# Kernel tuning notes

Hardware: AMD Instinct MI355X
Metric: run time of the kernel (lower is better)

The kernel has to match this reference:

```python
import jax, jax.numpy as jnp
import numpy as np

NUM_HEADS = 12


def _attend(q, k, v, scale):
    # q: [B,H,Q,D], k/v: [B,H,K,D]
    attn = jnp.einsum('bhqd,bhkd->bhqk', q, k) * scale
    attn = jax.nn.softmax(attn, axis=-1)
    return jnp.einsum('bhqk,bhkd->bhqd', attn, v)


def setup_inputs() -> dict:
    key = jax.random.key(0)
    k1, k2, k3 = jax.random.split(key, 3)
    B, N, C = 32, 1009, 768
    x = jax.random.normal(k1, (B, N, C), dtype=jnp.float32)
    W_qkv = jax.random.normal(k2, (C, 3 * C), dtype=jnp.float32) * (C ** -0.5)
    b_qkv = jnp.zeros((3 * C,), dtype=jnp.float32)
    W_proj = jax.random.normal(k3, (C, C), dtype=jnp.float32) * (C ** -0.5)
    b_proj = jnp.zeros((C,), dtype=jnp.float32)
    return {"x": x, "W_qkv": W_qkv, "b_qkv": b_qkv, "W_proj": W_proj,
            "b_proj": b_proj, "query_len": 1, "lens_z": 432}


def reference(x, W_qkv, b_qkv, W_proj, b_proj, query_len, lens_z):
    B, N, C = x.shape
    H = NUM_HEADS
    D = C // H
    scale = D ** -0.5
    lens_x = N - query_len - lens_z

    qkv = (x @ W_qkv + b_qkv).reshape(B, N, 3, H, D)
    qkv = jnp.transpose(qkv, (2, 0, 3, 1, 4))  # [3,B,H,N,D]
    q, k, v = qkv[0], qkv[1], qkv[2]

    sl_p = slice(0, query_len)
    sl_t = slice(query_len, query_len + lens_z)
    sl_s = slice(query_len + lens_z, N)

    # prompt: local self-attention
    x_prompt = _attend(q[:, :, sl_p], k[:, :, sl_p], v[:, :, sl_p], scale)
    # template: local self-attention
    x_template = _attend(q[:, :, sl_t], k[:, :, sl_t], v[:, :, sl_t], scale)
    # search: global attention over all tokens
    x_search = _attend(q[:, :, sl_s], k, v, scale)

    def merge(y, L):
        return jnp.transpose(y, (0, 2, 1, 3)).reshape(B, L, C)

    out = jnp.concatenate([merge(x_prompt, query_len),
                           merge(x_template, lens_z),
                           merge(x_search, lens_x)], axis=1)
    return out @ W_proj + b_proj
```

## Files before the change

kernel.cpp:

```cpp
#include <hip/hip_runtime.h>

#define B_ 32
#define N_ 1009
#define C_ 768
#define H_ 12
#define D_ 64
#define M_ (B_*N_)
#define MT_ 253
#define MPAD_ (MT_*128)
#define NKV_ 1024

typedef __attribute__((ext_vector_type(4))) float f32x4;
typedef __attribute__((ext_vector_type(8))) short s16x8;

__device__ __forceinline__ unsigned short f2bf(float f) {
  union { float f; unsigned u; } x; x.f = f;
  unsigned r = x.u + 0x7fffu + ((x.u >> 16) & 1u);
  return (unsigned short)(r >> 16);
}

__device__ __forceinline__ f32x4 mfma16(s16x8 a, s16x8 b, f32x4 c) {
  return __builtin_amdgcn_mfma_f32_16x16x32_bf16(a, b, c, 0, 0, 0);
}

__device__ __forceinline__ void async16(const void* g, void* l) {
  __builtin_amdgcn_global_load_lds((const __attribute__((address_space(1))) void*)g,
                                   (__attribute__((address_space(3))) void*)l, 16, 0, 0);
}

__device__ __forceinline__ float exp2_fast(float x) {
  float r; asm("v_exp_f32 %0, %1" : "=v"(r) : "v"(x)); return r;
}

__device__ __forceinline__ unsigned cvt_pk_bf16(float lo, float hi) {
  unsigned r; asm("v_cvt_pk_bf16_f32 %0, %1, %2" : "=v"(r) : "v"(lo), "v"(hi)); return r;
}

template<int NWG>
__device__ __forceinline__ int xcd_swz(int bid) {
  constexpr int q = NWG >> 3, r = NWG & 7;
  const int x = bid & 7, l = bid >> 3;
  return (x < r ? x * (q + 1) : r * (q + 1) + (x - r) * q) + l;
}

__global__ void prep(const float* __restrict__ x, unsigned short* __restrict__ xb,
                     const float* __restrict__ W_qkv, unsigned short* __restrict__ wqkvT,
                     const float* __restrict__ W_proj, unsigned short* __restrict__ wprojT,
                     unsigned short* __restrict__ kb, unsigned short* __restrict__ vt) {
  __shared__ float tile[64][65];
  int blk = blockIdx.x;

  if (blk < 12144) {
    const long e = ((long)blk * 256 + threadIdx.x) * 8;
    const long row = e / 768;
    s16x8 v;
    if (row < M_) {
#pragma unroll
      for (int j = 0; j < 8; ++j) v[j] = (short)f2bf(x[e + j]);
    } else {
      v = (s16x8){0,0,0,0,0,0,0,0};
    }
    *(s16x8*)&xb[e] = v;
    return;
  }
  blk -= 12144;

  if (blk < 432 + 144) {
    const float* in;
    unsigned short* out;
    int R, Ccols, bx, by;
    if (blk < 432) { in = W_qkv;  out = wqkvT;  R = 768; Ccols = 2304; bx = blk % 36;  by = blk / 36; }
    else { const int b2 = blk - 432;
           in = W_proj; out = wprojT; R = 768; Ccols = 768;  bx = b2 % 12;   by = b2 / 12; }
    const int tc = bx * 64, tr = by * 64;
#pragma unroll
    for (int i = 0; i < 16; ++i) {
      const int e = i * 256 + threadIdx.x;
      const int r = e >> 6, c = e & 63;
      tile[r][c] = in[(long)(tr + r) * Ccols + tc + c];
    }
    __syncthreads();
#pragma unroll
    for (int i = 0; i < 16; ++i) {
      const int e = i * 256 + threadIdx.x;
      const int c = e >> 6, r = e & 63;
      out[(long)(tc + c) * R + tr + r] = f2bf(tile[r][c]);
    }
    return;
  }
  blk -= 576;

  const int t = blk * 256 + threadIdx.x;
  if (t >= 368640) return;
  const int d = t & 63;
  const int r = t >> 6;
  const int bh = r / 15, tok = 1009 + (r - bh * 15);
  kb[(((long)bh << 10) + tok) * 64 + d] = 0;
  const int c = t % 15, row = t / 15;
  vt[((long)row << 10) + 1009 + c] = 0;
}

template<int MODE>
__global__ __launch_bounds__(256, 3)
void gemm_bt(const unsigned short* __restrict__ A,
             const unsigned short* __restrict__ Bt,
             const float* __restrict__ bias,
             unsigned short* __restrict__ qo,
             unsigned short* __restrict__ ko,
             unsigned short* __restrict__ vo,
             float* __restrict__ fo) {
  __shared__ __align__(16) unsigned short smem[24576];
  const int tid = threadIdx.x;
  const int lane = tid & 63;
  const int wv = tid >> 6;
  constexpr int NBN = (MODE == 0) ? 18 : 6;
  const int swzid = xcd_swz<MT_ * NBN>(blockIdx.x);
  const int bm = swzid / NBN;
  const int bn = swzid - bm * NBN;
  const int row0 = bm * 128;
  const int col0 = bn * 128;
  const int wr = (wv >> 1) * 64;
  const int wc = (wv & 1) * 64;

  auto stage = [&](int slot, int kt) {
#pragma unroll
    for (int c = 0; c < 2; ++c) {
      const int lds_off = c * 4096 + wv * 1024;
      const int gg = c * 256 + wv * 64 + lane;
      const int row = gg >> 2;
      const int ck = ((gg & 3) ^ ((row >> 1) & 3)) << 3;
      async16(A + (long)(row0 + row) * 768 + kt + ck, (char*)smem + slot * 16384 + lds_off);
      async16(Bt + (long)(col0 + row) * 768 + kt + ck, (char*)smem + slot * 16384 + 8192 + lds_off);
    }
  };

  f32x4 acc[4][4] = {};
  stage(0, 0);
  stage(1, 32);
  for (int it = 0; it < 24; ++it) {
    const int sl = it % 3;
    if (it + 1 < 24) {
      asm volatile("s_waitcnt vmcnt(4)" ::: "memory");
    } else {
      asm volatile("s_waitcnt vmcnt(0)" ::: "memory");
    }
    __builtin_amdgcn_s_barrier();
    if (it + 2 < 24) stage((it + 2) % 3, (it + 2) * 32);

    const unsigned short* Asb = smem + sl * 8192;
    const unsigned short* Bsb = Asb + 4096;
    s16x8 af[4], bfr[4];
#pragma unroll
    for (int m = 0; m < 4; ++m) {
      const int rA = wr + m * 16 + (lane & 15);
      af[m] = *(const s16x8*)&Asb[rA * 32 + (((lane >> 4) ^ ((rA >> 1) & 3)) << 3)];
    }
#pragma unroll
    for (int n = 0; n < 4; ++n) {
      const int rB = wc + n * 16 + (lane & 15);
      bfr[n] = *(const s16x8*)&Bsb[rB * 32 + (((lane >> 4) ^ ((rB >> 1) & 3)) << 3)];
    }
    __builtin_amdgcn_s_setprio(1);
#pragma unroll
    for (int m = 0; m < 4; ++m)
#pragma unroll
      for (int n = 0; n < 4; ++n)
        acc[m][n] = mfma16(af[m], bfr[n], acc[m][n]);
    __builtin_amdgcn_s_setprio(0);
  }
  __syncthreads();

  if (MODE == 0 && col0 < 1536) {
    const int qsel = col0 < 768;
#pragma unroll
    for (int m = 0; m < 4; ++m)
#pragma unroll
      for (int j = 0; j < 4; ++j)
#pragma unroll
        for (int n = 0; n < 4; ++n) {
          const int tk = wr + m * 16 + (lane >> 4) * 4 + j;
          const int cl = wc + n * 16 + (lane & 15);
          float val = acc[m][n][j] + bias[col0 + cl];
          if (qsel) val *= 0.18033688011112042f;
          smem[tk * 136 + cl] = f2bf(val);
        }
    __syncthreads();
    unsigned short* const dst = qsel ? qo : ko;
    const int colb = col0 - (qsel ? 0 : 768);
#pragma unroll
    for (int it = 0; it < 8; ++it) {
      const int g = it * 256 + tid;
      const int tk = g >> 4;
      const int ch = (g & 15) * 8;
      const int grow = row0 + tk;
      if (grow < M_) {
        const s16x8 vv = *(const s16x8*)&smem[tk * 136 + ch];
        const int b = grow / N_;
        const int ntok = grow - b * N_;
        const int rem = colb + ch;
        const int h = rem >> 6, d = rem & 63;
        *(s16x8*)&dst[(((((long)b * H_ + h) << 10) + ntok) << 6) + d] = vv;
      }
    }
    return;
  }

  if (MODE == 0) {
#pragma unroll
    for (int m = 0; m < 4; ++m)
#pragma unroll
      for (int j = 0; j < 4; ++j)
#pragma unroll
        for (int n = 0; n < 4; ++n) {
          const int dl = wc + n * 16 + (lane & 15);
          const int tk = wr + m * 16 + (lane >> 4) * 4 + j;
          smem[dl * 136 + tk] = f2bf(acc[m][n][j] + bias[col0 + dl]);
        }
    __syncthreads();
    const int h0 = (col0 - 1536) >> 6;
    const int b0 = row0 / N_;
    const int split = (b0 + 1) * N_ - row0;
#pragma unroll
    for (int it = 0; it < 8; ++it) {
      const int g = it * 256 + tid;
      const int dl = g >> 4;
      const int t8 = (g & 15) * 8;
      const s16x8 vv = *(const s16x8*)&smem[dl * 136 + t8];
      const int hh = h0 + (dl >> 6), dd = dl & 63;
#pragma unroll
      for (int jj = 0; jj < 8; ++jj) {
        const int tkb = t8 + jj;
        const int grow = row0 + tkb;
        if (grow < M_) {
          const int bb = (tkb < split) ? b0 : b0 + 1;
          const int ntok = grow - bb * N_;
          vo[(((((long)bb * H_ + hh) << 6) + dd) << 10) + ntok] = (unsigned short)vv[jj];
        }
      }
    }
    return;
  }

#pragma unroll
  for (int m = 0; m < 4; ++m) {
#pragma unroll
    for (int j = 0; j < 4; ++j) {
      const int grow = row0 + wr + m * 16 + (lane >> 4) * 4 + j;
      if (grow < M_) {
#pragma unroll
        for (int n = 0; n < 4; ++n) {
          const int col = col0 + wc + n * 16 + (lane & 15);
          fo[(long)grow * 768 + col] = acc[m][n][j] + bias[col];
        }
      }
    }
  }
}

__global__ __launch_bounds__(256, 4)
void attn_kernel(const unsigned short* __restrict__ qg,
                 const unsigned short* __restrict__ kg,
                 const unsigned short* __restrict__ vtg,
                 unsigned short* __restrict__ og) {
  __shared__ __align__(16) unsigned short Ks[2][64 * 64];
  __shared__ __align__(16) unsigned short Vts[2][64 * 64];
  __shared__ __align__(16) unsigned short Ps[64 * 64];

  const int bid = blockIdx.x;
  const int swz = (bid & 7) * 768 + (bid >> 3);
  const int tile = swz & 15;
  const int bh = swz >> 4;
  const int b = bh / H_;
  const int h = bh - b * H_;
  int qbase, qend, kstart, ktiles, kend;
  if (tile < 7) { qbase = 1 + 64 * tile;       qend = 433;  kstart = 1; ktiles = 7;  kend = 433; }
  else          { qbase = 433 + 64 * (tile-7); qend = 1009; kstart = 0; ktiles = 16; kend = 1009; }
  const long base  = (long)bh << 10;
  const long vbase = (long)bh << 6;
  const int tid = threadIdx.x, lane = tid & 63, wv = tid >> 6;
  const int q15 = lane & 15, q7 = lane & 7, g = lane >> 4;

  if (tile == 7 && tid < 64)
    og[((long)b * N_) * 768 + h * 64 + tid] = vtg[(vbase + tid) << 10];

  s16x8 qa[2];
  {
    const unsigned short* qp = qg + (base + qbase + wv * 16 + q15) * 64;
    qa[0] = *(const s16x8*)(qp + g * 8);
    qa[1] = *(const s16x8*)(qp + 32 + g * 8);
  }
  asm volatile("s_waitcnt vmcnt(0)" ::: "memory");

  f32x4 o[4] = {};
  float mrow = -1e30f, lrow = 0.f;

  auto stage = [&](int bufsel, int kb0) {
#pragma unroll
    for (int it = 0; it < 2; ++it) {
      const int ldsoff = (it * 256 + wv * 64) * 16;
      const int gr = it * 256 + wv * 64 + lane;
      const int rl = gr >> 3;
      const int cs = (gr & 7) ^ (rl & 7);
      async16(kg + ((base + kb0 + rl) << 6) + cs * 8, (char*)&Ks[bufsel][0] + ldsoff);
      async16(vtg + ((vbase + rl) << 10) + kb0 + cs * 8, (char*)&Vts[bufsel][0] + ldsoff);
    }
  };

  const int prow = wv * 16 + q15;

  stage(0, kstart);
  for (int kt = 0; kt < ktiles; ++kt) {
    const int buf = kt & 1;
    const int kbase0 = kstart + 64 * kt;
    if (kt + 1 < ktiles) {
      stage(buf ^ 1, kbase0 + 64);
      asm volatile("s_waitcnt vmcnt(4)" ::: "memory");
    } else {
      asm volatile("s_waitcnt vmcnt(0)" ::: "memory");
    }
    __builtin_amdgcn_s_barrier();

    f32x4 s4[4];
    __builtin_amdgcn_s_setprio(1);
#pragma unroll
    for (int n = 0; n < 4; ++n) {
      const int krow = n * 16 + q15;
      const int r7 = krow & 7;
      f32x4 a = {};
      a = mfma16(*(const s16x8*)&Ks[buf][krow * 64 + ((g ^ r7) << 3)],       qa[0], a);
      a = mfma16(*(const s16x8*)&Ks[buf][krow * 64 + (((4 + g) ^ r7) << 3)], qa[1], a);
      s4[n] = a;
    }
    __builtin_amdgcn_s_setprio(0);

    if (kbase0 + 64 > kend) {
#pragma unroll
      for (int n = 0; n < 4; ++n)
#pragma unroll
        for (int j = 0; j < 4; ++j)
          if (kbase0 + n * 16 + g * 4 + j >= kend) s4[n][j] = -1e30f;
    }

    float rmax = fmaxf(
        fmaxf(fmaxf(fmaxf(s4[0][0], s4[0][1]), fmaxf(s4[0][2], s4[0][3])),
              fmaxf(fmaxf(s4[1][0], s4[1][1]), fmaxf(s4[1][2], s4[1][3]))),
        fmaxf(fmaxf(fmaxf(s4[2][0], s4[2][1]), fmaxf(s4[2][2], s4[2][3])),
              fmaxf(fmaxf(s4[3][0], s4[3][1]), fmaxf(s4[3][2], s4[3][3]))));
    rmax = fmaxf(rmax, __shfl_xor(rmax, 16));
    rmax = fmaxf(rmax, __shfl_xor(rmax, 32));

    if (!__all(rmax <= mrow + 8.f)) {
      const float mnew = fmaxf(mrow, rmax);
      const float corr = exp2_fast(mrow - mnew);
      mrow = mnew;
      lrow *= corr;
#pragma unroll
      for (int f = 0; f < 4; ++f)
#pragma unroll
        for (int j = 0; j < 4; ++j) o[f][j] *= corr;
    }
    const float mnew = mrow;

    float psum = 0.f;
#pragma unroll
    for (int n = 0; n < 4; ++n) {
#pragma unroll
      for (int j = 0; j < 4; ++j) {
        s4[n][j] = exp2_fast(s4[n][j] - mnew);
        psum += s4[n][j];
      }
      uint2 pw;
      pw.x = cvt_pk_bf16(s4[n][0], s4[n][1]);
      pw.y = cvt_pk_bf16(s4[n][2], s4[n][3]);
      *(uint2*)((char*)Ps + prow * 128 + (((n * 2 + (g >> 1)) ^ q7) << 4) + (g & 1) * 8) = pw;
    }
    psum += __shfl_xor(psum, 16);
    psum += __shfl_xor(psum, 32);
    lrow += psum;

    s16x8 pa[2];
#pragma unroll
    for (int kf = 0; kf < 2; ++kf)
      pa[kf] = *(const s16x8*)((char*)Ps + prow * 128 + (((kf * 4 + g) ^ q7) << 4));
    __builtin_amdgcn_s_setprio(1);
#pragma unroll
    for (int f = 0; f < 4; ++f) {
      const int vrow = f * 16 + q15;
      const int v7 = vrow & 7;
#pragma unroll
      for (int kf = 0; kf < 2; ++kf) {
        const s16x8 vb = *(const s16x8*)&Vts[buf][vrow * 64 + (((kf * 4 + g) ^ v7) << 3)];
        o[f] = mfma16(vb, pa[kf], o[f]);
      }
    }
    __builtin_amdgcn_s_setprio(0);

    asm volatile("s_waitcnt lgkmcnt(0)" ::: "memory");
    __builtin_amdgcn_s_barrier();
  }

  const int qrow = qbase + wv * 16 + q15;
  if (qrow < qend) {
    const float inv = 1.0f / lrow;
    unsigned short* op = og + ((long)b * N_ + qrow) * 768 + h * 64 + g * 4;
#pragma unroll
    for (int f = 0; f < 4; ++f) {
      uint2 ow;
      ow.x = cvt_pk_bf16(o[f][0] * inv, o[f][1] * inv);
      ow.y = cvt_pk_bf16(o[f][2] * inv, o[f][3] * inv);
      *(uint2*)(op + f * 16) = ow;
    }
  }
}

extern "C" void kernel_launch(void* const* d_in, const int* in_sizes, int n_in,
                              void* d_out, int out_size, void* d_ws, size_t ws_size,
                              hipStream_t stream) {
  const float* x      = (const float*)d_in[0];
  const float* W_qkv  = (const float*)d_in[1];
  const float* b_qkv  = (const float*)d_in[2];
  const float* W_proj = (const float*)d_in[3];
  const float* b_proj = (const float*)d_in[4];
  float* out = (float*)d_out;

  unsigned short* ws = (unsigned short*)d_ws;
  unsigned short* wqkvT  = ws;
  unsigned short* wprojT = wqkvT + (long)2304 * 768;
  unsigned short* qb = wprojT + (long)768 * 768;
  const long kvsz = (long)B_ * H_ * NKV_ * D_;
  unsigned short* kb = qb + kvsz;
  unsigned short* vb = kb + kvsz;
  unsigned short* xb = vb + kvsz;
  unsigned short* attnout = xb;

  prep<<<14160, 256, 0, stream>>>(x, xb, W_qkv, wqkvT, W_proj, wprojT, kb, vb);
  gemm_bt<0><<<MT_ * 18, 256, 0, stream>>>(xb, wqkvT, b_qkv, qb, kb, vb, nullptr);
  attn_kernel<<<B_ * H_ * 16, 256, 0, stream>>>(qb, kb, vb, attnout);
  gemm_bt<1><<<MT_ * 6, 256, 0, stream>>>(attnout, wprojT, b_proj, nullptr, nullptr, nullptr, out);
}
```

Before: 393.6 us.

## Process two query tiles per attention block to share K/V tile loads

Each attention workgroup now handles two 64-row query tiles against the same staged K/V tiles, which halves K/V global loads and LDS staging per query. The grid shrinks from 16 to 9 blocks per (batch, head). Odd tile counts are covered by having the last slot compute the same tile twice and write identical results. The cost is doubled accumulator and Q registers, some redundant compute on the duplicated tiles, and fewer blocks available to fill the GPU.

```diff
diff --git a/kernel.cpp b/kernel.cpp
--- a/kernel.cpp
+++ b/kernel.cpp
@@ -267,32 +267,39 @@
   __shared__ __align__(16) unsigned short Ps[64 * 64];
 
   const int bid = blockIdx.x;
-  const int swz = (bid & 7) * 768 + (bid >> 3);
-  const int tile = swz & 15;
-  const int bh = swz >> 4;
+  const int swz = (bid & 7) * 432 + (bid >> 3);
+  const int bh = swz / 9;
+  const int slot = swz - bh * 9;
   const int b = bh / H_;
   const int h = bh - b * H_;
-  int qbase, qend, kstart, ktiles, kend;
-  if (tile < 7) { qbase = 1 + 64 * tile;       qend = 433;  kstart = 1; ktiles = 7;  kend = 433; }
-  else          { qbase = 433 + 64 * (tile-7); qend = 1009; kstart = 0; ktiles = 16; kend = 1009; }
+  int kstart, ktiles, kend, qt0, qt1;
+  if (slot < 4) { kstart = 1; ktiles = 7;  kend = 433;
+                  qt0 = slot * 2;      qt1 = (slot < 3) ? qt0 + 1 : 6; }
+  else          { kstart = 0; ktiles = 16; kend = 1009; const int s2 = slot - 4;
+                  qt0 = 7 + s2 * 2;    qt1 = (s2 < 4) ? qt0 + 1 : 15; }
+  const int qb0 = (qt0 < 7) ? 1 + 64 * qt0 : 433 + 64 * (qt0 - 7);
+  const int qb1 = (qt1 < 7) ? 1 + 64 * qt1 : 433 + 64 * (qt1 - 7);
   const long base  = (long)bh << 10;
   const long vbase = (long)bh << 6;
   const int tid = threadIdx.x, lane = tid & 63, wv = tid >> 6;
   const int q15 = lane & 15, q7 = lane & 7, g = lane >> 4;
 
-  if (tile == 7 && tid < 64)
+  if (slot == 4 && tid < 64)
     og[((long)b * N_) * 768 + h * 64 + tid] = vtg[(vbase + tid) << 10];
 
-  s16x8 qa[2];
+  s16x8 qa0[2], qa1[2];
   {
-    const unsigned short* qp = qg + (base + qbase + wv * 16 + q15) * 64;
-    qa[0] = *(const s16x8*)(qp + g * 8);
-    qa[1] = *(const s16x8*)(qp + 32 + g * 8);
+    const unsigned short* qp0 = qg + (base + qb0 + wv * 16 + q15) * 64;
+    qa0[0] = *(const s16x8*)(qp0 + g * 8);
+    qa0[1] = *(const s16x8*)(qp0 + 32 + g * 8);
+    const unsigned short* qp1 = qg + (base + qb1 + wv * 16 + q15) * 64;
+    qa1[0] = *(const s16x8*)(qp1 + g * 8);
+    qa1[1] = *(const s16x8*)(qp1 + 32 + g * 8);
   }
   asm volatile("s_waitcnt vmcnt(0)" ::: "memory");
 
-  f32x4 o[4] = {};
-  float mrow = -1e30f, lrow = 0.f;
+  f32x4 o0[4] = {}, o1[4] = {};
+  float m0 = -1e30f, l0 = 0.f, m1 = -1e30f, l1 = 0.f;
 
   auto stage = [&](int bufsel, int kb0) {
 #pragma unroll
@@ -307,6 +314,84 @@
   };
 
   const int prow = wv * 16 + q15;
+
+  auto half = [&](const s16x8* qa, f32x4* o, float& mrow, float& lrow,
+                  int buf, int kbase0) {
+    f32x4 s4[4];
+    __builtin_amdgcn_s_setprio(1);
+#pragma unroll
+    for (int n = 0; n < 4; ++n) {
+      const int krow = n * 16 + q15;
+      const int r7 = krow & 7;
+      f32x4 a = {};
+      a = mfma16(*(const s16x8*)&Ks[buf][krow * 64 + ((g ^ r7) << 3)],       qa[0], a);
+      a = mfma16(*(const s16x8*)&Ks[buf][krow * 64 + (((4 + g) ^ r7) << 3)], qa[1], a);
+      s4[n] = a;
+    }
+    __builtin_amdgcn_s_setprio(0);
+
+    if (kbase0 + 64 > kend) {
+#pragma unroll
+      for (int n = 0; n < 4; ++n)
+#pragma unroll
+        for (int j = 0; j < 4; ++j)
+          if (kbase0 + n * 16 + g * 4 + j >= kend) s4[n][j] = -1e30f;
+    }
+
+    float rmax = fmaxf(
+        fmaxf(fmaxf(fmaxf(s4[0][0], s4[0][1]), fmaxf(s4[0][2], s4[0][3])),
+              fmaxf(fmaxf(s4[1][0], s4[1][1]), fmaxf(s4[1][2], s4[1][3]))),
+        fmaxf(fmaxf(fmaxf(s4[2][0], s4[2][1]), fmaxf(s4[2][2], s4[2][3])),
+              fmaxf(fmaxf(s4[3][0], s4[3][1]), fmaxf(s4[3][2], s4[3][3]))));
+    rmax = fmaxf(rmax, __shfl_xor(rmax, 16));
+    rmax = fmaxf(rmax, __shfl_xor(rmax, 32));
+
+    if (!__all(rmax <= mrow + 8.f)) {
+      const float mnew = fmaxf(mrow, rmax);
+      const float corr = exp2_fast(mrow - mnew);
+      mrow = mnew;
+      lrow *= corr;
+#pragma unroll
+      for (int f = 0; f < 4; ++f)
+#pragma unroll
+        for (int j = 0; j < 4; ++j) o[f][j] *= corr;
+    }
+    const float mnew = mrow;
+
+    float psum = 0.f;
+#pragma unroll
+    for (int n = 0; n < 4; ++n) {
+#pragma unroll
+      for (int j = 0; j < 4; ++j) {
+        s4[n][j] = exp2_fast(s4[n][j] - mnew);
+        psum += s4[n][j];
+      }
+      uint2 pw;
+      pw.x = cvt_pk_bf16(s4[n][0], s4[n][1]);
+      pw.y = cvt_pk_bf16(s4[n][2], s4[n][3]);
+      *(uint2*)((char*)Ps + prow * 128 + (((n * 2 + (g >> 1)) ^ q7) << 4) + (g & 1) * 8) = pw;
+    }
+    psum += __shfl_xor(psum, 16);
+    psum += __shfl_xor(psum, 32);
+    lrow += psum;
+
+    s16x8 pa[2];
+#pragma unroll
+    for (int kf = 0; kf < 2; ++kf)
+      pa[kf] = *(const s16x8*)((char*)Ps + prow * 128 + (((kf * 4 + g) ^ q7) << 4));
+    __builtin_amdgcn_s_setprio(1);
+#pragma unroll
+    for (int f = 0; f < 4; ++f) {
+      const int vrow = f * 16 + q15;
+      const int v7 = vrow & 7;
+#pragma unroll
+      for (int kf = 0; kf < 2; ++kf) {
+        const s16x8 vb = *(const s16x8*)&Vts[buf][vrow * 64 + (((kf * 4 + g) ^ v7) << 3)];
+        o[f] = mfma16(vb, pa[kf], o[f]);
+      }
+    }
+    __builtin_amdgcn_s_setprio(0);
+  };
 
   stage(0, kstart);
   for (int kt = 0; kt < ktiles; ++kt) {
@@ -320,95 +405,39 @@
     }
     __builtin_amdgcn_s_barrier();
 
-    f32x4 s4[4];
-    __builtin_amdgcn_s_setprio(1);
-#pragma unroll
-    for (int n = 0; n < 4; ++n) {
-      const int krow = n * 16 + q15;
-      const int r7 = krow & 7;
-      f32x4 a = {};
-      a = mfma16(*(const s16x8*)&Ks[buf][krow * 64 + ((g ^ r7) << 3)],       qa[0], a);
-      a = mfma16(*(const s16x8*)&Ks[buf][krow * 64 + (((4 + g) ^ r7) << 3)], qa[1], a);
-      s4[n] = a;
-    }
-    __builtin_amdgcn_s_setprio(0);
-
-    if (kbase0 + 64 > kend) {
-#pragma unroll
-      for (int n = 0; n < 4; ++n)
-#pragma unroll
-        for (int j = 0; j < 4; ++j)
-          if (kbase0 + n * 16 + g * 4 + j >= kend) s4[n][j] = -1e30f;
-    }
-
-    float rmax = fmaxf(
-        fmaxf(fmaxf(fmaxf(s4[0][0], s4[0][1]), fmaxf(s4[0][2], s4[0][3])),
-              fmaxf(fmaxf(s4[1][0], s4[1][1]), fmaxf(s4[1][2], s4[1][3]))),
-        fmaxf(fmaxf(fmaxf(s4[2][0], s4[2][1]), fmaxf(s4[2][2], s4[2][3])),
-              fmaxf(fmaxf(s4[3][0], s4[3][1]), fmaxf(s4[3][2], s4[3][3]))));
-    rmax = fmaxf(rmax, __shfl_xor(rmax, 16));
-    rmax = fmaxf(rmax, __shfl_xor(rmax, 32));
-
-    if (!__all(rmax <= mrow + 8.f)) {
-      const float mnew = fmaxf(mrow, rmax);
-      const float corr = exp2_fast(mrow - mnew);
-      mrow = mnew;
-      lrow *= corr;
-#pragma unroll
-      for (int f = 0; f < 4; ++f)
-#pragma unroll
-        for (int j = 0; j < 4; ++j) o[f][j] *= corr;
-    }
-    const float mnew = mrow;
-
-    float psum = 0.f;
-#pragma unroll
-    for (int n = 0; n < 4; ++n) {
-#pragma unroll
-      for (int j = 0; j < 4; ++j) {
-        s4[n][j] = exp2_fast(s4[n][j] - mnew);
-        psum += s4[n][j];
-      }
-      uint2 pw;
-      pw.x = cvt_pk_bf16(s4[n][0], s4[n][1]);
-      pw.y = cvt_pk_bf16(s4[n][2], s4[n][3]);
-      *(uint2*)((char*)Ps + prow * 128 + (((n * 2 + (g >> 1)) ^ q7) << 4) + (g & 1) * 8) = pw;
-    }
-    psum += __shfl_xor(psum, 16);
-    psum += __shfl_xor(psum, 32);
-    lrow += psum;
-
-    s16x8 pa[2];
-#pragma unroll
-    for (int kf = 0; kf < 2; ++kf)
-      pa[kf] = *(const s16x8*)((char*)Ps + prow * 128 + (((kf * 4 + g) ^ q7) << 4));
-    __builtin_amdgcn_s_setprio(1);
-#pragma unroll
-    for (int f = 0; f < 4; ++f) {
-      const int vrow = f * 16 + q15;
-      const int v7 = vrow & 7;
-#pragma unroll
-      for (int kf = 0; kf < 2; ++kf) {
-        const s16x8 vb = *(const s16x8*)&Vts[buf][vrow * 64 + (((kf * 4 + g) ^ v7) << 3)];
-        o[f] = mfma16(vb, pa[kf], o[f]);
-      }
-    }
-    __builtin_amdgcn_s_setprio(0);
+    half(qa0, o0, m0, l0, buf, kbase0);
+    half(qa1, o1, m1, l1, buf, kbase0);
 
     asm volatile("s_waitcnt lgkmcnt(0)" ::: "memory");
     __builtin_amdgcn_s_barrier();
   }
 
-  const int qrow = qbase + wv * 16 + q15;
-  if (qrow < qend) {
-    const float inv = 1.0f / lrow;
-    unsigned short* op = og + ((long)b * N_ + qrow) * 768 + h * 64 + g * 4;
-#pragma unroll
-    for (int f = 0; f < 4; ++f) {
-      uint2 ow;
-      ow.x = cvt_pk_bf16(o[f][0] * inv, o[f][1] * inv);
-      ow.y = cvt_pk_bf16(o[f][2] * inv, o[f][3] * inv);
-      *(uint2*)(op + f * 16) = ow;
+  {
+    const int qrow = qb0 + wv * 16 + q15;
+    if (qrow < (qt0 < 7 ? 433 : 1009)) {
+      const float inv = 1.0f / l0;
+      unsigned short* op = og + ((long)b * N_ + qrow) * 768 + h * 64 + g * 4;
+#pragma unroll
+      for (int f = 0; f < 4; ++f) {
+        uint2 ow;
+        ow.x = cvt_pk_bf16(o0[f][0] * inv, o0[f][1] * inv);
+        ow.y = cvt_pk_bf16(o0[f][2] * inv, o0[f][3] * inv);
+        *(uint2*)(op + f * 16) = ow;
+      }
+    }
+  }
+  {
+    const int qrow = qb1 + wv * 16 + q15;
+    if (qrow < (qt1 < 7 ? 433 : 1009)) {
+      const float inv = 1.0f / l1;
+      unsigned short* op = og + ((long)b * N_ + qrow) * 768 + h * 64 + g * 4;
+#pragma unroll
+      for (int f = 0; f < 4; ++f) {
+        uint2 ow;
+        ow.x = cvt_pk_bf16(o1[f][0] * inv, o1[f][1] * inv);
+        ow.y = cvt_pk_bf16(o1[f][2] * inv, o1[f][3] * inv);
+        *(uint2*)(op + f * 16) = ow;
+      }
     }
   }
 }
@@ -435,6 +464,6 @@
 
   prep<<<14160, 256, 0, stream>>>(x, xb, W_qkv, wqkvT, W_proj, wprojT, kb, vb);
   gemm_bt<0><<<MT_ * 18, 256, 0, stream>>>(xb, wqkvT, b_qkv, qb, kb, vb, nullptr);
-  attn_kernel<<<B_ * H_ * 16, 256, 0, stream>>>(qb, kb, vb, attnout);
+  attn_kernel<<<B_ * H_ * 9, 256, 0, stream>>>(qb, kb, vb, attnout);
   gemm_bt<1><<<MT_ * 6, 256, 0, stream>>>(attnout, wprojT, b_proj, nullptr, nullptr, nullptr, out);
 }
```

After: 389.9 us, median of 2. Within noise of the previous version (-0.9%).
